# Optimization experiments

Hardware: AMD Instinct MI355X
Metric: run time of the kernel (lower is better)

Reference implementation:

```python
import jax, jax.numpy as jnp
import numpy as np

B, T, H, K = 4, 1024, 1024, 16
HD = H // K  # head dim
EPS = 1e-5


def _layernorm(x, g, b):
    mu = jnp.mean(x, axis=-1, keepdims=True)
    var = jnp.mean(jnp.square(x - mu), axis=-1, keepdims=True)
    return (x - mu) * jax.lax.rsqrt(var + EPS) * g + b


def setup_inputs() -> dict:
    key = jax.random.key(0)
    ks = jax.random.split(key, 16)
    s = 0.02
    return {
        "x": jax.random.normal(ks[0], (B, T, H), jnp.float32),
        "ln1_g": jnp.ones((H,), jnp.float32),
        "ln1_b": jnp.zeros((H,), jnp.float32),
        "ln2_g": jnp.ones((H,), jnp.float32),
        "ln2_b": jnp.zeros((H,), jnp.float32),
        "Wq": jax.random.normal(ks[1], (H, H), jnp.float32) * s,
        "bq": jnp.zeros((H,), jnp.float32),
        "Wk": jax.random.normal(ks[2], (H, H), jnp.float32) * s,
        "bk": jnp.zeros((H,), jnp.float32),
        "Wv": jax.random.normal(ks[3], (H, H), jnp.float32) * s,
        "bv": jnp.zeros((H,), jnp.float32),
        "W1": jax.random.normal(ks[4], (H, 4 * H), jnp.float32) * s,
        "b1": jnp.zeros((4 * H,), jnp.float32),
        "W2": jax.random.normal(ks[5], (4 * H, H), jnp.float32) * s,
        "b2": jnp.zeros((H,), jnp.float32),
    }


def reference(x, ln1_g, ln1_b, ln2_g, ln2_b, Wq, bq, Wk, bk, Wv, bv, W1, b1, W2, b2):
    # --- attention sub-block ---
    h = _layernorm(x, ln1_g, ln1_b)                      # (B,T,H)
    q = (h @ Wq + bq).reshape(B, T, K, HD).transpose(0, 2, 1, 3)  # (B,K,T,hd)
    k = (h @ Wk + bk).reshape(B, T, K, HD).transpose(0, 2, 1, 3)
    v = (h @ Wv + bv).reshape(B, T, K, HD).transpose(0, 2, 1, 3)
    qkt = jnp.einsum('bkqd,bkpd->bkqp', q, k)            # (B,K,T,T)
    attn = qkt * (1.0 / np.sqrt(HD))
    # module quirk: masked positions are FILLED with 1e-9 (not -inf) before softmax
    causal_mask = jnp.triu(jnp.ones((T, T), bool), k=1)  # True above diagonal = masked
    attn = jnp.where(causal_mask, jnp.float32(1e-9), attn)
    attn = jax.nn.softmax(attn, axis=-1)
    y = jnp.einsum('bkqp,bkpd->bkqd', attn, v)           # (B,K,T,hd)
    y = y.transpose(0, 2, 1, 3).reshape(B, T, H)
    x = x + y
    # --- MLP sub-block (dropout is identity at eval) ---
    h2 = _layernorm(x, ln2_g, ln2_b)
    m = jax.nn.gelu(h2 @ W1 + b1, approximate=False) @ W2 + b2
    return x + m
```

## Files before the change

### kernel.cpp

```cpp
#include <hip/hip_runtime.h>
#include <hip/hip_bf16.h>
#include <math.h>


typedef __attribute__((ext_vector_type(8))) short bf16x8;
typedef __attribute__((ext_vector_type(4))) float f32x4;

#define DEVINL __device__ __forceinline__

#define LOG2E_SCALE 0.18033688f
#define MASK2 1.4426950408889634e-9f

DEVINL void stage16(const __hip_bfloat16* g, short* l) {
  __builtin_amdgcn_global_load_lds(
      (const __attribute__((address_space(1))) unsigned int*)g,
      (__attribute__((address_space(3))) unsigned int*)l, 16, 0, 0);
}

DEVINL float bf2f(short u) {
  unsigned x = ((unsigned)(unsigned short)u) << 16;
  float f; __builtin_memcpy(&f, &x, 4); return f;
}

DEVINL short f2bf_s(float f) {
  __hip_bfloat16 h = __float2bfloat16(f);
  short s; __builtin_memcpy(&s, &h, 2); return s;
}

DEVINL float block_sum(float v, float* sb) {
  #pragma unroll
  for (int o = 32; o; o >>= 1) v += __shfl_down(v, o);
  const int lane = threadIdx.x & 63, w = threadIdx.x >> 6;
  if (lane == 0) sb[w] = v;
  __syncthreads();
  float r = sb[0] + sb[1] + sb[2] + sb[3];
  __syncthreads();
  return r;
}

template<int BM, int BN, int WM, int WN>
DEVINL void gemm_core64(const __hip_bfloat16* __restrict__ A, int lda,
                        const __hip_bfloat16* __restrict__ Bt, int ldb,
                        int Kd, int row0, int col0,
                        f32x4 (&acc)[WM/16][WN/16],
                        short* lds_a, short* lds_b) {
  constexpr int MI = WM / 16, NI = WN / 16, WNC = BN / WN;
  constexpr int CA = BM * 8, CB = BN * 8;
  const int tid = threadIdx.x;
  const int lane = tid & 63, wave = tid >> 6;
  const int wm = (wave / WNC) * WM, wn = (wave % WNC) * WN;
  const int lr = lane & 15, lq = lane >> 4;
  for (int k0 = 0; k0 < Kd; k0 += 64) {
    #pragma unroll
    for (int c = tid; c < CA; c += 256) {
      const int r = c >> 3, kc = ((c & 7) ^ (r & 7)) << 3;
      stage16(A + (size_t)(row0 + r) * lda + k0 + kc, lds_a + c * 8);
    }
    #pragma unroll
    for (int c = tid; c < CB; c += 256) {
      const int r = c >> 3, kc = ((c & 7) ^ (r & 7)) << 3;
      stage16(Bt + (size_t)(col0 + r) * ldb + k0 + kc, lds_b + c * 8);
    }
    __syncthreads();
    #pragma unroll
    for (int s = 0; s < 2; s++) {
      bf16x8 af[MI], bfr[NI];
      #pragma unroll
      for (int mi = 0; mi < MI; mi++) {
        const int m = wm + mi * 16 + lr;
        af[mi] = *(const bf16x8*)(lds_a + m * 64 + (((s * 4 + lq) ^ (m & 7)) << 3));
      }
      #pragma unroll
      for (int ni = 0; ni < NI; ni++) {
        const int n = wn + ni * 16 + lr;
        bfr[ni] = *(const bf16x8*)(lds_b + n * 64 + (((s * 4 + lq) ^ (n & 7)) << 3));
      }
      #pragma unroll
      for (int mi = 0; mi < MI; mi++)
        #pragma unroll
        for (int ni = 0; ni < NI; ni++)
          acc[mi][ni] = __builtin_amdgcn_mfma_f32_16x16x32_bf16(
              af[mi], bfr[ni], acc[mi][ni], 0, 0, 0);
    }
    __syncthreads();
  }
}

__global__ __launch_bounds__(256) void k_tcvt(const float* __restrict__ src,
                                              __hip_bfloat16* __restrict__ dst,
                                              int R, int C, int dstOff, int dstPitch) {
  __shared__ float tile[32][33];
  const int c0 = blockIdx.x * 32, r0 = blockIdx.y * 32;
  const int tx = threadIdx.x, ty = threadIdx.y;
  #pragma unroll
  for (int i = 0; i < 32; i += 8)
    tile[ty + i][tx] = src[(size_t)(r0 + ty + i) * C + c0 + tx];
  __syncthreads();
  #pragma unroll
  for (int i = 0; i < 32; i += 8)
    dst[(size_t)(c0 + ty + i + dstOff) * dstPitch + r0 + tx] =
        __float2bfloat16(tile[tx][ty + i]);
}

__global__ __launch_bounds__(256) void k_tcvt3(const float* __restrict__ Wq,
                                               const float* __restrict__ Wk,
                                               const float* __restrict__ Wv,
                                               __hip_bfloat16* __restrict__ dst) {
  __shared__ float tile[32][33];
  const float* src = blockIdx.z == 0 ? Wq : (blockIdx.z == 1 ? Wk : Wv);
  const int dstOff = blockIdx.z << 10;
  const int c0 = blockIdx.x * 32, r0 = blockIdx.y * 32;
  const int tx = threadIdx.x, ty = threadIdx.y;
  #pragma unroll
  for (int i = 0; i < 32; i += 8)
    tile[ty + i][tx] = src[(size_t)(r0 + ty + i) * 1024 + c0 + tx];
  __syncthreads();
  #pragma unroll
  for (int i = 0; i < 32; i += 8)
    dst[(size_t)(c0 + ty + i + dstOff) * 1024 + r0 + tx] =
        __float2bfloat16(tile[tx][ty + i]);
}

__global__ __launch_bounds__(256) void k_pack_bias(const float* __restrict__ bq,
                                                   const float* __restrict__ bk,
                                                   const float* __restrict__ bv,
                                                   float* __restrict__ o) {
  const int i = blockIdx.x * 256 + threadIdx.x;
  if (i < 3072)
    o[i] = i < 1024 ? bq[i] : (i < 2048 ? bk[i - 1024] : bv[i - 2048]);
}

__global__ __launch_bounds__(256) void k_ln(const float* __restrict__ x,
                                            const float* __restrict__ y,
                                            const float* __restrict__ g,
                                            const float* __restrict__ bb,
                                            __hip_bfloat16* __restrict__ o,
                                            const float* __restrict__ badd,
                                            float* __restrict__ oinit) {
  __shared__ float sb[4];
  const int t = threadIdx.x;
  const size_t base = (size_t)blockIdx.x * 1024 + t * 4;
  const int c = t * 4;
  float4 xv = *(const float4*)(x + base);
  if (y) {
    float4 yv = *(const float4*)(y + base);
    xv.x += yv.x; xv.y += yv.y; xv.z += yv.z; xv.w += yv.w;
    float4 ov;
    ov.x = xv.x + badd[c + 0]; ov.y = xv.y + badd[c + 1];
    ov.z = xv.z + badd[c + 2]; ov.w = xv.w + badd[c + 3];
    *(float4*)(oinit + base) = ov;
  }
  const float mu = block_sum(xv.x + xv.y + xv.z + xv.w, sb) * (1.f / 1024.f);
  const float dx = xv.x - mu, dy = xv.y - mu, dz = xv.z - mu, dw = xv.w - mu;
  const float var = block_sum(dx * dx + dy * dy + dz * dz + dw * dw, sb) * (1.f / 1024.f);
  const float rs = rsqrtf(var + 1e-5f);
  o[base + 0] = __float2bfloat16(dx * rs * g[c + 0] + bb[c + 0]);
  o[base + 1] = __float2bfloat16(dy * rs * g[c + 1] + bb[c + 1]);
  o[base + 2] = __float2bfloat16(dz * rs * g[c + 2] + bb[c + 2]);
  o[base + 3] = __float2bfloat16(dw * rs * g[c + 3] + bb[c + 3]);
}

__global__ __launch_bounds__(256) void k_gemm_qkv(
    const __hip_bfloat16* __restrict__ h1, const __hip_bfloat16* __restrict__ Wt,
    const float* __restrict__ bqkv, __hip_bfloat16* __restrict__ Q,
    __hip_bfloat16* __restrict__ K, __hip_bfloat16* __restrict__ Vt) {
  __shared__ alignas(16) short smem[16896];
  short* la = smem;
  short* lb = smem + 8192;
  short* lc = smem;
  const int row0 = blockIdx.x * 128, col0 = blockIdx.y * 128;
  f32x4 acc[4][4] = {};
  gemm_core64<128, 128, 64, 64>(h1, 1024, Wt, 1024, 1024, row0, col0, acc, la, lb);
  const int tid = threadIdx.x, lane = tid & 63, wave = tid >> 6;
  const int wm = (wave >> 1) * 64, wn = (wave & 1) * 64, lr = lane & 15, lq = lane >> 4;
  const int which = col0 >> 10;
  const int h0 = (col0 & 1023) >> 6;
  const int b = row0 >> 10, t0 = row0 & 1023;
  if (which < 2) {
    const float qs = (which == 0) ? LOG2E_SCALE : 1.f;
    #pragma unroll
    for (int mi = 0; mi < 4; mi++)
      #pragma unroll
      for (int ni = 0; ni < 4; ni++)
        #pragma unroll
        for (int r = 0; r < 4; r++) {
          const int row = wm + mi * 16 + lq * 4 + r;
          const int col = wn + ni * 16 + lr;
          lc[row * 132 + col] = f2bf_s((acc[mi][ni][r] + bqkv[col0 + col]) * qs);
        }
    __syncthreads();
    __hip_bfloat16* O = which == 0 ? Q : K;
    #pragma unroll
    for (int c = 0; c < 8; c++) {
      const int f = tid + 256 * c;
      const int r = f >> 4, cc = f & 15;
      const int col = cc * 8;
      const int head = h0 + (col >> 6), d = col & 63;
      float4 vv = *(const float4*)(lc + r * 132 + col);
      *(float4*)(O + (((size_t)(b * 16 + head)) << 16) + (t0 + r) * 64 + d) = vv;
    }
  } else {
    #pragma unroll
    for (int mi = 0; mi < 4; mi++)
      #pragma unroll
      for (int ni = 0; ni < 4; ni++)
        #pragma unroll
        for (int r = 0; r < 4; r++) {
          const int row = wm + mi * 16 + lq * 4 + r;
          const int col = wn + ni * 16 + lr;
          lc[col * 132 + row] = f2bf_s(acc[mi][ni][r] + bqkv[col0 + col]);
        }
    __syncthreads();
    #pragma unroll
    for (int c = 0; c < 8; c++) {
      const int f = tid + 256 * c;
      const int dl = f >> 4, tc = f & 15;
      const int head = h0 + (dl >> 6), d = dl & 63;
      float4 vv = *(const float4*)(lc + dl * 132 + tc * 8);
      *(float4*)(Vt + (((size_t)(b * 16 + head)) << 16) + (size_t)d * 1024 +
                 t0 + tc * 8) = vv;
    }
  }
}

__global__ __launch_bounds__(256) void k_tailv(const __hip_bfloat16* __restrict__ Vt,
                                               float* __restrict__ TV) {
  __shared__ float ts[8][64];
  const int hb = blockIdx.x, tid = threadIdx.x;
  const __hip_bfloat16* Vh = Vt + ((size_t)hb << 16);
  for (int w = tid; w < 512; w += 256) {
    const int kt = w >> 6, d = w & 63;
    const short* p = (const short*)(Vh + (size_t)d * 1024 + kt * 128);
    float s = 0.f;
    for (int j = 0; j < 128; j += 8) {
      bf16x8 v = *(const bf16x8*)(p + j);
      #pragma unroll
      for (int e = 0; e < 8; e++) s += bf2f(v[e]);
    }
    ts[kt][d] = s;
  }
  __syncthreads();
  for (int w = tid; w < 512; w += 256) {
    const int qt = w >> 6, d = w & 63;
    float s = 0.f;
    for (int kt = qt + 1; kt < 8; kt++) s += ts[kt][d];
    TV[((size_t)hb * 8 + qt) * 64 + d] = s;
  }
}

__global__ __launch_bounds__(256, 3) void k_attn(
    const __hip_bfloat16* __restrict__ Q, const __hip_bfloat16* __restrict__ K,
    const __hip_bfloat16* __restrict__ Vt, const float* __restrict__ TV,
    float* __restrict__ y) {
  __shared__ short lp[64 * 130];
  __shared__ short lK[128 * 64];
  __shared__ short lV[128 * 64];
  const int hb = blockIdx.y;
  const int j = (blockIdx.y & 32) ? (15 - (int)blockIdx.x) : (int)blockIdx.x;
  const int q0 = j * 64;
  const int nkt = (j >> 1) + 1;
  const int tid = threadIdx.x, lane = tid & 63, wave = tid >> 6;
  const int lr = lane & 15, lq = lane >> 4;
  const int wm = wave * 16;
  const __hip_bfloat16* Qh = Q + ((size_t)hb << 16);
  const __hip_bfloat16* Kh = K + ((size_t)hb << 16);
  const __hip_bfloat16* Vh = Vt + ((size_t)hb << 16);

  bf16x8 qf[2];
  #pragma unroll
  for (int s = 0; s < 2; s++)
    qf[s] = *(const bf16x8*)((const short*)Qh +
                             (size_t)(q0 + wm + lr) * 64 + s * 32 + lq * 8);

  f32x4 oacc[4] = {};
  float mrow[4], lrow[4];
  #pragma unroll
  for (int r = 0; r < 4; r++) { mrow[r] = -1e30f; lrow[r] = 0.f; }

  for (int c = tid; c < 1024; c += 256)
    stage16(Kh + (size_t)(c >> 3) * 64 + (((c & 7) ^ ((c >> 3) & 7)) << 3),
            lK + c * 8);
  __syncthreads();

  for (int kt = 0; kt < nkt; kt++) {
    const int k0 = kt * 128;
    f32x4 sacc[8] = {};
    __builtin_amdgcn_s_setprio(1);
    #pragma unroll
    for (int s = 0; s < 2; s++) {
      bf16x8 bf[8];
      #pragma unroll
      for (int ni = 0; ni < 8; ni++) {
        const int n = ni * 16 + lr;
        bf[ni] = *(const bf16x8*)(lK + n * 64 + (((s * 4 + lq) ^ (n & 7)) << 3));
      }
      #pragma unroll
      for (int ni = 0; ni < 8; ni++)
        sacc[ni] = __builtin_amdgcn_mfma_f32_16x16x32_bf16(
            qf[s], bf[ni], sacc[ni], 0, 0, 0);
    }
    __builtin_amdgcn_s_setprio(0);
    __syncthreads();
    for (int c = tid; c < 1024; c += 256)
      stage16(Vh + (size_t)(c >> 4) * 1024 + k0 + (((c & 15) ^ ((c >> 4) & 15)) << 3),
              lV + c * 8);
    if (kt + 1 < nkt) {
      const int k1 = k0 + 128;
      for (int c = tid; c < 1024; c += 256)
        stage16(Kh + (size_t)(k1 + (c >> 3)) * 64 + (((c & 7) ^ ((c >> 3) & 7)) << 3),
                lK + c * 8);
    }
    const bool last = (kt == nkt - 1);
    #pragma unroll
    for (int r = 0; r < 4; r++) {
      const int grow = q0 + wm + lq * 4 + r;
      float tmax = -1e30f;
      #pragma unroll
      for (int ni = 0; ni < 8; ni++) {
        float v = sacc[ni][r];
        if (last && (k0 + ni * 16 + lr) > grow) v = MASK2;
        sacc[ni][r] = v;
        tmax = fmaxf(tmax, v);
      }
      #pragma unroll
      for (int msk = 8; msk; msk >>= 1) tmax = fmaxf(tmax, __shfl_xor(tmax, msk));
      const float mn = fmaxf(mrow[r], tmax);
      const float al = __builtin_amdgcn_exp2f(mrow[r] - mn);
      float rs = 0.f;
      #pragma unroll
      for (int ni = 0; ni < 8; ni++) {
        const float pv = __builtin_amdgcn_exp2f(sacc[ni][r] - mn);
        sacc[ni][r] = pv;
        rs += pv;
      }
      #pragma unroll
      for (int msk = 8; msk; msk >>= 1) rs += __shfl_xor(rs, msk);
      mrow[r] = mn;
      lrow[r] = lrow[r] * al + rs;
      #pragma unroll
      for (int ni = 0; ni < 4; ni++) oacc[ni][r] *= al;
    }
    #pragma unroll
    for (int r = 0; r < 4; r++) {
      const int row = wm + lq * 4 + r;
      #pragma unroll
      for (int ni = 0; ni < 8; ni++)
        lp[row * 130 + ni * 16 + lr] = f2bf_s(sacc[ni][r]);
    }
    __syncthreads();
    __builtin_amdgcn_s_setprio(1);
    #pragma unroll
    for (int ks = 0; ks < 4; ks++) {
      bf16x8 pa, vb[4];
      pa = *(const bf16x8*)(lp + (wm + lr) * 130 + ks * 32 + lq * 8);
      #pragma unroll
      for (int ni = 0; ni < 4; ni++) {
        const int d = ni * 16 + lr;
        vb[ni] = *(const bf16x8*)(lV + d * 128 + (((ks * 4 + lq) ^ (d & 15)) << 3));
      }
      #pragma unroll
      for (int ni = 0; ni < 4; ni++)
        oacc[ni] = __builtin_amdgcn_mfma_f32_16x16x32_bf16(
            pa, vb[ni], oacc[ni], 0, 0, 0);
    }
    __builtin_amdgcn_s_setprio(0);
  }

  const int b = hb >> 4, h = hb & 15;
  const float cv = (float)(1024 - nkt * 128);
  const float* tv = TV + ((size_t)hb * 8 + (j >> 1)) * 64;
  #pragma unroll
  for (int r = 0; r < 4; r++) {
    const int t = q0 + wm + lq * 4 + r;
    const float tail = __builtin_amdgcn_exp2f(MASK2 - mrow[r]);
    const float inv = 1.f / (lrow[r] + cv * tail);
    #pragma unroll
    for (int ni = 0; ni < 4; ni++) {
      const int d = ni * 16 + lr;
      y[((size_t)(b * 1024 + t) << 10) + h * 64 + d] =
          (oacc[ni][r] + tail * tv[d]) * inv;
    }
  }
}

template<int MH, int NH>
DEVINL void ph_read(const short* pa, const short* pb, int wr, int wc,
                    int lr, int lq, bf16x8 (&af)[4][2], bf16x8 (&bf)[2][2]) {
  if (NH == 0) {
    #pragma unroll
    for (int mi2 = 0; mi2 < 4; mi2++)
      #pragma unroll
      for (int ks = 0; ks < 2; ks++) {
        const int r = wr * 128 + MH * 64 + mi2 * 16 + lr;
        af[mi2][ks] = *(const bf16x8*)(pa + r * 64 + (((ks * 4 + lq) ^ (r & 7)) << 3));
      }
  }
  #pragma unroll
  for (int ni2 = 0; ni2 < 2; ni2++)
    #pragma unroll
    for (int ks = 0; ks < 2; ks++) {
      const int n = wc * 64 + NH * 32 + ni2 * 16 + lr;
      bf[ni2][ks] = *(const bf16x8*)(pb + n * 64 + (((ks * 4 + lq) ^ (n & 7)) << 3));
    }
}

DEVINL void ph_sync() {
  __builtin_amdgcn_s_barrier();
  asm volatile("s_waitcnt lgkmcnt(0)" ::: "memory");
  __builtin_amdgcn_sched_barrier(0);
}

template<int MH, int NH>
DEVINL void ph_mfma(f32x4 (&acc)[8][4], bf16x8 (&af)[4][2], bf16x8 (&bf)[2][2]) {
  __builtin_amdgcn_s_setprio(1);
  #pragma unroll
  for (int mi2 = 0; mi2 < 4; mi2++)
    #pragma unroll
    for (int ni2 = 0; ni2 < 2; ni2++)
      #pragma unroll
      for (int ks = 0; ks < 2; ks++)
        acc[MH * 4 + mi2][NH * 2 + ni2] = __builtin_amdgcn_mfma_f32_16x16x32_bf16(
            af[mi2][ks], bf[ni2][ks], acc[MH * 4 + mi2][NH * 2 + ni2], 0, 0, 0);
  __builtin_amdgcn_s_setprio(0);
  __builtin_amdgcn_s_barrier();
}

__global__ __launch_bounds__(512, 2) void k_gemm_mlp1(const __hip_bfloat16* __restrict__ h2,
                                                      const __hip_bfloat16* __restrict__ W1t,
                                                      const float* __restrict__ b1,
                                                      __hip_bfloat16* __restrict__ G) {
  __shared__ alignas(16) short smem[65536];
  short* Ae = smem;
  short* Ao = smem + 16384;
  short* Be = smem + 32768;
  short* Bo = smem + 49152;
  const int row0 = blockIdx.x * 256, col0 = blockIdx.y * 256;
  const int tid = threadIdx.x, lane = tid & 63, wid = tid >> 6;
  const int lr = lane & 15, lq = lane >> 4;
  const int wr = wid >> 2, wc = wid & 3;
  const __hip_bfloat16* A = h2 + (size_t)row0 * 1024;
  const __hip_bfloat16* Bt = W1t + (size_t)col0 * 1024;

  auto STG = [&](const __hip_bfloat16* src, int k0, int h, short* dst, int SH) {
    #pragma unroll
    for (int ii = 0; ii < 2; ii++) {
      const int f = tid + ii * 512;
      const int rp = f >> 3, P = f & 7;
      const int r = ((rp >> SH) << (SH + 1)) | (h << SH) | (rp & ((1 << SH) - 1));
      const int g = P ^ (r & 7);
      stage16(src + (size_t)r * 1024 + k0 + g * 8, dst + r * 64 + P * 8);
    }
  };

  f32x4 acc[8][4] = {};
  bf16x8 af[4][2], bf[2][2];

  STG(A, 0, 0, Ae, 6);  STG(Bt, 0, 0, Be, 5);
  STG(A, 0, 1, Ae, 6);  STG(Bt, 0, 1, Be, 5);
  STG(A, 64, 0, Ao, 6); STG(Bt, 64, 0, Bo, 5);
  asm volatile("s_waitcnt vmcnt(4)" ::: "memory");
  __syncthreads();

  for (int i = 0; i < 8; ++i) {
    const int kE1 = (i + 1) * 128;
    const int kO0 = i * 128 + 64;
    const int kO1 = kE1 + 64;
    const bool more = (i + 1 < 8);
    ph_read<0, 0>(Ae, Be, wr, wc, lr, lq, af, bf);
    STG(A, kO0, 1, Ao, 6);
    ph_sync();
    ph_mfma<0, 0>(acc, af, bf);
    ph_read<0, 1>(Ae, Be, wr, wc, lr, lq, af, bf);
    STG(Bt, kO0, 1, Bo, 5);
    ph_sync();
    ph_mfma<0, 1>(acc, af, bf);
    ph_read<1, 0>(Ae, Be, wr, wc, lr, lq, af, bf);
    if (more) STG(A, kE1, 0, Ae, 6);
    ph_sync();
    ph_mfma<1, 0>(acc, af, bf);
    ph_read<1, 1>(Ae, Be, wr, wc, lr, lq, af, bf);
    if (more) {
      STG(Bt, kE1, 0, Be, 5);
      asm volatile("s_waitcnt vmcnt(4)" ::: "memory");
    } else {
      asm volatile("s_waitcnt vmcnt(0)" ::: "memory");
    }
    ph_sync();
    ph_mfma<1, 1>(acc, af, bf);
    ph_read<0, 0>(Ao, Bo, wr, wc, lr, lq, af, bf);
    if (more) STG(A, kE1, 1, Ae, 6);
    ph_sync();
    ph_mfma<0, 0>(acc, af, bf);
    ph_read<0, 1>(Ao, Bo, wr, wc, lr, lq, af, bf);
    if (more) STG(Bt, kE1, 1, Be, 5);
    ph_sync();
    ph_mfma<0, 1>(acc, af, bf);
    ph_read<1, 0>(Ao, Bo, wr, wc, lr, lq, af, bf);
    if (more) STG(A, kO1, 0, Ao, 6);
    ph_sync();
    ph_mfma<1, 0>(acc, af, bf);
    ph_read<1, 1>(Ao, Bo, wr, wc, lr, lq, af, bf);
    if (more) {
      STG(Bt, kO1, 0, Bo, 5);
      asm volatile("s_waitcnt vmcnt(4)" ::: "memory");
    }
    ph_sync();
    ph_mfma<1, 1>(acc, af, bf);
  }

  short* lc = smem;
  #pragma unroll
  for (int pr = 0; pr < 4; pr++) {
    if ((wid >> 2) == (pr >> 1)) {
      const int mib = (pr & 1) * 4;
      #pragma unroll
      for (int mi2 = 0; mi2 < 4; mi2++)
        #pragma unroll
        for (int ni = 0; ni < 4; ni++)
          #pragma unroll
          for (int rr = 0; rr < 4; rr++) {
            const int rloc = mi2 * 16 + lq * 4 + rr;
            const int col = (wid & 3) * 64 + ni * 16 + lr;
            float v = acc[mib + mi2][ni][rr] + b1[col0 + col];
            const float u2 = fminf(v * (2.3022079f + 0.1029434f * v * v), 80.f);
            const float e = __builtin_amdgcn_exp2f(u2);
            v = v * e * __builtin_amdgcn_rcpf(e + 1.f);
            lc[rloc * 264 + col] = f2bf_s(v);
          }
    }
    __syncthreads();
    #pragma unroll
    for (int c = 0; c < 4; c++) {
      const int f = tid + 512 * c;
      const int r = f >> 5, cc = f & 31;
      float4 vv = *(const float4*)(lc + r * 264 + cc * 8);
      *(float4*)(G + ((size_t)(row0 + pr * 64 + r) << 12) + col0 + cc * 8) = vv;
    }
    __syncthreads();
  }
}

template<int MH>
DEVINL void mm2(f32x4 (&acc)[4][4], bf16x8 (&af)[2][2], bf16x8 (&bf)[4][2]) {
  __builtin_amdgcn_s_setprio(1);
  #pragma unroll
  for (int mi2 = 0; mi2 < 2; mi2++)
    #pragma unroll
    for (int ni = 0; ni < 4; ni++)
      #pragma unroll
      for (int ks = 0; ks < 2; ks++)
        acc[MH * 2 + mi2][ni] = __builtin_amdgcn_mfma_f32_16x16x32_bf16(
            af[mi2][ks], bf[ni][ks], acc[MH * 2 + mi2][ni], 0, 0, 0);
  __builtin_amdgcn_s_setprio(0);
  __builtin_amdgcn_s_barrier();
}

__global__ __launch_bounds__(512, 2) void k_gemm_mlp2(const __hip_bfloat16* __restrict__ G,
                                                      const __hip_bfloat16* __restrict__ W2t,
                                                      float* __restrict__ out) {
  __shared__ alignas(16) short smem[49152];
  short* Ae = smem;
  short* Ao = smem + 16384;
  short* Be = smem + 32768;
  short* Bo = smem + 40960;
  const int row0 = blockIdx.x * 256, col0 = blockIdx.y * 128;
  const int kOff = blockIdx.z * 2048;
  const int tid = threadIdx.x, lane = tid & 63, wid = tid >> 6;
  const int lr = lane & 15, lq = lane >> 4;
  const int wr = wid >> 1, wc = wid & 1;
  const __hip_bfloat16* A = G + (size_t)row0 * 4096 + kOff;
  const __hip_bfloat16* Bt = W2t + (size_t)col0 * 4096 + kOff;

  auto STGA = [&](int k0, int h, short* dst) {
    #pragma unroll
    for (int ii = 0; ii < 2; ii++) {
      const int f = tid + ii * 512;
      const int rp = f >> 3, P = f & 7;
      const int r = ((rp >> 5) << 6) | (h << 5) | (rp & 31);
      const int g = P ^ (r & 7);
      stage16(A + (size_t)r * 4096 + k0 + g * 8, dst + r * 64 + P * 8);
    }
  };
  auto STGB = [&](int k0, short* dst) {
    #pragma unroll
    for (int ii = 0; ii < 2; ii++) {
      const int f = tid + ii * 512;
      const int r = f >> 3, P = f & 7;
      const int g = P ^ (r & 7);
      stage16(Bt + (size_t)r * 4096 + k0 + g * 8, dst + r * 64 + P * 8);
    }
  };

  f32x4 acc[4][4] = {};
  bf16x8 af[2][2], bf[4][2];

  auto RDA = [&](const short* pa, int MH) {
    #pragma unroll
    for (int mi2 = 0; mi2 < 2; mi2++)
      #pragma unroll
      for (int ks = 0; ks < 2; ks++) {
        const int r = wr * 64 + MH * 32 + mi2 * 16 + lr;
        af[mi2][ks] = *(const bf16x8*)(pa + r * 64 + (((ks * 4 + lq) ^ (r & 7)) << 3));
      }
  };
  auto RDB = [&](const short* pb) {
    #pragma unroll
    for (int ni = 0; ni < 4; ni++)
      #pragma unroll
      for (int ks = 0; ks < 2; ks++) {
        const int n = wc * 64 + ni * 16 + lr;
        bf[ni][ks] = *(const bf16x8*)(pb + n * 64 + (((ks * 4 + lq) ^ (n & 7)) << 3));
      }
  };

  STGB(0, Be); STGA(0, 0, Ae);
  STGA(0, 1, Ae);
  STGB(64, Bo); STGA(64, 0, Ao);
  asm volatile("s_waitcnt vmcnt(4)" ::: "memory");
  __syncthreads();

  for (int i = 0; i < 16; ++i) {
    const int kE1 = (i + 1) * 128, kO0 = i * 128 + 64, kO1 = kE1 + 64;
    const bool more = (i + 1 < 16);
    RDA(Ae, 0); RDB(Be);
    STGA(kO0, 1, Ao);
    asm volatile("s_waitcnt vmcnt(2)" ::: "memory");
    ph_sync();
    mm2<0>(acc, af, bf);
    RDA(Ae, 1);
    if (more) { STGB(kE1, Be); STGA(kE1, 0, Ae); }
    ph_sync();
    mm2<1>(acc, af, bf);
    RDA(Ao, 0); RDB(Bo);
    if (more) {
      STGA(kE1, 1, Ae);
      asm volatile("s_waitcnt vmcnt(6)" ::: "memory");
    } else {
      asm volatile("s_waitcnt vmcnt(0)" ::: "memory");
    }
    ph_sync();
    mm2<0>(acc, af, bf);
    RDA(Ao, 1);
    if (more) {
      STGB(kO1, Bo); STGA(kO1, 0, Ao);
      asm volatile("s_waitcnt vmcnt(4)" ::: "memory");
    }
    ph_sync();
    mm2<1>(acc, af, bf);
  }

  #pragma unroll
  for (int mi = 0; mi < 4; mi++)
    #pragma unroll
    for (int ni = 0; ni < 4; ni++)
      #pragma unroll
      for (int rr = 0; rr < 4; rr++) {
        const int grow = row0 + wr * 64 + mi * 16 + lq * 4 + rr;
        const int gcol = col0 + wc * 64 + ni * 16 + lr;
        atomicAdd(out + (((size_t)grow << 10) + gcol), acc[mi][ni][rr]);
      }
}

extern "C" void kernel_launch(void* const* d_in, const int* in_sizes, int n_in,
                              void* d_out, int out_size, void* d_ws, size_t ws_size,
                              hipStream_t stream) {
  const float* x     = (const float*)d_in[0];
  const float* ln1_g = (const float*)d_in[1];
  const float* ln1_b = (const float*)d_in[2];
  const float* ln2_g = (const float*)d_in[3];
  const float* ln2_b = (const float*)d_in[4];
  const float* Wq    = (const float*)d_in[5];
  const float* bq    = (const float*)d_in[6];
  const float* Wk    = (const float*)d_in[7];
  const float* bk    = (const float*)d_in[8];
  const float* Wv    = (const float*)d_in[9];
  const float* bv    = (const float*)d_in[10];
  const float* W1    = (const float*)d_in[11];
  const float* b1    = (const float*)d_in[12];
  const float* W2    = (const float*)d_in[13];
  const float* b2    = (const float*)d_in[14];
  float* out = (float*)d_out;

  char* p = (char*)d_ws;
  auto alloc = [&](size_t bytes) { char* r = p; p += (bytes + 255) & ~(size_t)255; return r; };
  __hip_bfloat16* wqkv = (__hip_bfloat16*)alloc(3072 * 1024 * 2);
  __hip_bfloat16* w1t  = (__hip_bfloat16*)alloc(4096 * 1024 * 2);
  __hip_bfloat16* w2t  = (__hip_bfloat16*)alloc(1024 * 4096 * 2);
  float*          bqkv = (float*)alloc(3072 * 4);
  __hip_bfloat16* h1   = (__hip_bfloat16*)alloc(4096 * 1024 * 2);
  __hip_bfloat16* Qb   = (__hip_bfloat16*)alloc((size_t)64 * 65536 * 2);
  __hip_bfloat16* Kb   = (__hip_bfloat16*)alloc((size_t)64 * 65536 * 2);
  __hip_bfloat16* Vt   = (__hip_bfloat16*)alloc((size_t)64 * 65536 * 2);
  float*          TV   = (float*)alloc((size_t)64 * 8 * 64 * 4);
  float*          yb   = (float*)alloc((size_t)4096 * 1024 * 4);
  __hip_bfloat16* h2   = (__hip_bfloat16*)alloc(4096 * 1024 * 2);
  __hip_bfloat16* G    = (__hip_bfloat16*)alloc((size_t)4096 * 4096 * 2);
  (void)ws_size; (void)in_sizes; (void)n_in; (void)out_size;

  const dim3 b256(256), bt(32, 8);
  k_tcvt3<<<dim3(32, 32, 3), bt, 0, stream>>>(Wq, Wk, Wv, wqkv);
  k_tcvt<<<dim3(128, 32), bt, 0, stream>>>(W1, w1t, 1024, 4096, 0, 1024);
  k_tcvt<<<dim3(32, 128), bt, 0, stream>>>(W2, w2t, 4096, 1024, 0, 4096);
  k_pack_bias<<<12, b256, 0, stream>>>(bq, bk, bv, bqkv);

  k_ln<<<4096, b256, 0, stream>>>(x, nullptr, ln1_g, ln1_b, h1, nullptr, nullptr);
  k_gemm_qkv<<<dim3(32, 24), b256, 0, stream>>>(h1, wqkv, bqkv, Qb, Kb, Vt);
  k_tailv<<<64, b256, 0, stream>>>(Vt, TV);
  k_attn<<<dim3(16, 64), b256, 0, stream>>>(Qb, Kb, Vt, TV, yb);

  k_ln<<<4096, b256, 0, stream>>>(x, yb, ln2_g, ln2_b, h2, b2, out);
  k_gemm_mlp1<<<dim3(16, 16), dim3(512), 0, stream>>>(h2, w1t, b1, G);
  k_gemm_mlp2<<<dim3(16, 8, 2), dim3(512), 0, stream>>>(G, w2t, out);
}
```

Measured before the change: 328.4 us.

## Replace split-K MLP2 GEMM with 128x128 tiles and plain stores

The second MLP GEMM moves from 256x128 tiles split two ways along K, which needed atomicAdd, to 128x128 tiles covering the full K range. This keeps the same 256-block count but lets each output element be written by one block with a plain read-add-write instead of an atomic. The warp layout becomes 2x4, shared memory shrinks, and the vmcnt waits are retuned for the new load counts. In exchange, per-block arithmetic intensity drops and the K loop doubles in length.

```diff
diff --git a/kernel.cpp b/kernel.cpp
--- a/kernel.cpp
+++ b/kernel.cpp
@@ -541,12 +541,12 @@
 }
 
 template<int MH>
-DEVINL void mm2(f32x4 (&acc)[4][4], bf16x8 (&af)[2][2], bf16x8 (&bf)[4][2]) {
+DEVINL void mmh(f32x4 (&acc)[4][2], bf16x8 (&af)[2][2], bf16x8 (&bf)[2][2]) {
   __builtin_amdgcn_s_setprio(1);
   #pragma unroll
   for (int mi2 = 0; mi2 < 2; mi2++)
     #pragma unroll
-    for (int ni = 0; ni < 4; ni++)
+    for (int ni = 0; ni < 2; ni++)
       #pragma unroll
       for (int ks = 0; ks < 2; ks++)
         acc[MH * 2 + mi2][ni] = __builtin_amdgcn_mfma_f32_16x16x32_bf16(
@@ -558,28 +558,23 @@
 __global__ __launch_bounds__(512, 2) void k_gemm_mlp2(const __hip_bfloat16* __restrict__ G,
                                                       const __hip_bfloat16* __restrict__ W2t,
                                                       float* __restrict__ out) {
-  __shared__ alignas(16) short smem[49152];
+  __shared__ alignas(16) short smem[32768];
   short* Ae = smem;
-  short* Ao = smem + 16384;
-  short* Be = smem + 32768;
-  short* Bo = smem + 40960;
-  const int row0 = blockIdx.x * 256, col0 = blockIdx.y * 128;
-  const int kOff = blockIdx.z * 2048;
+  short* Ao = smem + 8192;
+  short* Be = smem + 16384;
+  short* Bo = smem + 24576;
+  const int row0 = blockIdx.x * 128, col0 = blockIdx.y * 128;
   const int tid = threadIdx.x, lane = tid & 63, wid = tid >> 6;
   const int lr = lane & 15, lq = lane >> 4;
-  const int wr = wid >> 1, wc = wid & 1;
-  const __hip_bfloat16* A = G + (size_t)row0 * 4096 + kOff;
-  const __hip_bfloat16* Bt = W2t + (size_t)col0 * 4096 + kOff;
+  const int wr = wid >> 2, wc = wid & 3;
+  const __hip_bfloat16* A = G + (size_t)row0 * 4096;
+  const __hip_bfloat16* Bt = W2t + (size_t)col0 * 4096;
 
   auto STGA = [&](int k0, int h, short* dst) {
-    #pragma unroll
-    for (int ii = 0; ii < 2; ii++) {
-      const int f = tid + ii * 512;
-      const int rp = f >> 3, P = f & 7;
-      const int r = ((rp >> 5) << 6) | (h << 5) | (rp & 31);
-      const int g = P ^ (r & 7);
-      stage16(A + (size_t)r * 4096 + k0 + g * 8, dst + r * 64 + P * 8);
-    }
+    const int rp = tid >> 3, P = tid & 7;
+    const int r = ((rp >> 5) << 6) | (h << 5) | (rp & 31);
+    const int g = P ^ (r & 7);
+    stage16(A + (size_t)r * 4096 + k0 + g * 8, dst + r * 64 + P * 8);
   };
   auto STGB = [&](int k0, short* dst) {
     #pragma unroll
@@ -591,8 +586,8 @@
     }
   };
 
-  f32x4 acc[4][4] = {};
-  bf16x8 af[2][2], bf[4][2];
+  f32x4 acc[4][2] = {};
+  bf16x8 af[2][2], bf[2][2];
 
   auto RDA = [&](const short* pa, int MH) {
     #pragma unroll
@@ -605,10 +600,10 @@
   };
   auto RDB = [&](const short* pb) {
     #pragma unroll
-    for (int ni = 0; ni < 4; ni++)
+    for (int ni = 0; ni < 2; ni++)
       #pragma unroll
       for (int ks = 0; ks < 2; ks++) {
-        const int n = wc * 64 + ni * 16 + lr;
+        const int n = wc * 32 + ni * 16 + lr;
         bf[ni][ks] = *(const bf16x8*)(pb + n * 64 + (((ks * 4 + lq) ^ (n & 7)) << 3));
       }
   };
@@ -619,45 +614,51 @@
   asm volatile("s_waitcnt vmcnt(4)" ::: "memory");
   __syncthreads();
 
-  for (int i = 0; i < 16; ++i) {
+  for (int i = 0; i < 32; ++i) {
     const int kE1 = (i + 1) * 128, kO0 = i * 128 + 64, kO1 = kE1 + 64;
-    const bool more = (i + 1 < 16);
+    const bool more = (i + 1 < 32);
     RDA(Ae, 0); RDB(Be);
     STGA(kO0, 1, Ao);
-    asm volatile("s_waitcnt vmcnt(2)" ::: "memory");
-    ph_sync();
-    mm2<0>(acc, af, bf);
+    asm volatile("s_waitcnt vmcnt(4)" ::: "memory");
+    ph_sync();
+    mmh<0>(acc, af, bf);
     RDA(Ae, 1);
-    if (more) { STGB(kE1, Be); STGA(kE1, 0, Ae); }
-    ph_sync();
-    mm2<1>(acc, af, bf);
+    if (more) {
+      STGB(kE1, Be); STGA(kE1, 0, Ae);
+      asm volatile("s_waitcnt vmcnt(4)" ::: "memory");
+    } else {
+      asm volatile("s_waitcnt vmcnt(1)" ::: "memory");
+    }
+    ph_sync();
+    mmh<1>(acc, af, bf);
     RDA(Ao, 0); RDB(Bo);
     if (more) {
       STGA(kE1, 1, Ae);
-      asm volatile("s_waitcnt vmcnt(6)" ::: "memory");
+      asm volatile("s_waitcnt vmcnt(4)" ::: "memory");
     } else {
       asm volatile("s_waitcnt vmcnt(0)" ::: "memory");
     }
     ph_sync();
-    mm2<0>(acc, af, bf);
+    mmh<0>(acc, af, bf);
     RDA(Ao, 1);
     if (more) {
       STGB(kO1, Bo); STGA(kO1, 0, Ao);
       asm volatile("s_waitcnt vmcnt(4)" ::: "memory");
     }
     ph_sync();
-    mm2<1>(acc, af, bf);
+    mmh<1>(acc, af, bf);
   }
 
   #pragma unroll
   for (int mi = 0; mi < 4; mi++)
     #pragma unroll
-    for (int ni = 0; ni < 4; ni++)
+    for (int ni = 0; ni < 2; ni++)
       #pragma unroll
       for (int rr = 0; rr < 4; rr++) {
-        const int grow = row0 + wr * 64 + mi * 16 + lq * 4 + rr;
-        const int gcol = col0 + wc * 64 + ni * 16 + lr;
-        atomicAdd(out + (((size_t)grow << 10) + gcol), acc[mi][ni][rr]);
+        const int grow = row0 + wr * 64 + (mi >> 1) * 32 + (mi & 1) * 16 + lq * 4 + rr;
+        const int gcol = col0 + wc * 32 + ni * 16 + lr;
+        float* p = out + (((size_t)grow << 10) + gcol);
+        *p += acc[mi][ni][rr];
       }
 }
 
@@ -710,5 +711,5 @@
 
   k_ln<<<4096, b256, 0, stream>>>(x, yb, ln2_g, ln2_b, h2, b2, out);
   k_gemm_mlp1<<<dim3(16, 16), dim3(512), 0, stream>>>(h2, w1t, b1, G);
-  k_gemm_mlp2<<<dim3(16, 8, 2), dim3(512), 0, stream>>>(G, w2t, out);
-}
+  k_gemm_mlp2<<<dim3(32, 8), dim3(512), 0, stream>>>(G, w2t, out);
+}
```

Result: faster. 307.6 us (-6.3%).
